# Optimization experiments

Hardware: AMD Instinct MI355X
Metric: run time of the kernel (lower is better)

## Reference

```python
import jax, jax.numpy as jnp
import numpy as np

B, N, D = 8, 128, 256
EPS = 1e-5


def _layernorm(x, g, b):
    m = jnp.mean(x, axis=-1, keepdims=True)
    v = jnp.mean(jnp.square(x - m), axis=-1, keepdims=True)
    return (x - m) * jax.lax.rsqrt(v + EPS) * g + b


def setup_inputs() -> dict:
    key = jax.random.key(0)
    ks = jax.random.split(key, 24)
    s = 0.05  # param init scale
    return {
        "text": jax.random.normal(ks[0], (B, N, D), jnp.float32),
        "adj1": jax.random.uniform(ks[1], (B, N, N), jnp.float32),
        "adj2": jax.random.uniform(ks[2], (B, N, N), jnp.float32),
        "edge1": jax.random.normal(ks[3], (B, N, N, D), jnp.float32) * 0.1,
        "edge2": jax.random.normal(ks[4], (B, N, N, D), jnp.float32) * 0.1,
        "textmask": jnp.ones((B, N), jnp.float32),
        "weight": jax.random.normal(ks[5], (D, D), jnp.float32) * s,
        "bias": jax.random.normal(ks[6], (D,), jnp.float32) * s,
        "gamma": jnp.ones((D,), jnp.float32),
        "beta": jnp.zeros((D,), jnp.float32),
        "fuse1_w": jax.random.normal(ks[7], (2 * D, D), jnp.float32) * s,
        "fuse2_w": jax.random.normal(ks[8], (2 * D, D), jnp.float32) * s,
        "fc3_w": jax.random.normal(ks[9], (2 * D, D), jnp.float32) * s,
        "fc1_w0": jax.random.normal(ks[10], (3 * D, D), jnp.float32) * s,
        "fc1_w1": jax.random.normal(ks[11], (D, 1), jnp.float32) * s,
        "fc1_b1": jnp.zeros((1,), jnp.float32),
        "fc2_w0": jax.random.normal(ks[12], (3 * D, D), jnp.float32) * s,
        "fc2_w1": jax.random.normal(ks[13], (D, 1), jnp.float32) * s,
        "fc2_b1": jnp.zeros((1,), jnp.float32),
        "align_lin": jax.random.normal(ks[14], (D, D), jnp.float32) * s,
        "align_bias": jax.random.normal(ks[15], (D,), jnp.float32) * s,
    }


def reference(text, adj1, adj2, edge1, edge2, textmask, weight, bias, gamma,
              beta, fuse1_w, fuse2_w, fc3_w, fc1_w0, fc1_w1, fc1_b1,
              fc2_w0, fc2_w1, fc2_b1, align_lin, align_bias):
    d = text.shape[-1]
    # ---- SelfAlignment ----
    logits = jnp.einsum('bid,bjd->bij', text @ align_lin, text)
    mask_add = (1.0 - textmask)[:, None, :] * -1e20
    probs = jax.nn.softmax(logits + mask_add, axis=-1)
    outss = jnp.einsum('bij,bjd->bid', probs, text) * textmask[..., None] + align_bias

    # ---- GCN body ----
    out = jax.nn.relu(text @ weight)  # [B,N,D]

    # edge contributions are loop-invariant: precompute once
    # torch cat([x,e]) @ W  ==  x @ W[:d] + e @ W[d:]
    e1_fuse = jnp.einsum('bijd,de->bije', edge1, fuse1_w[d:])
    e2_fuse = jnp.einsum('bijd,de->bije', edge2, fuse2_w[d:])
    e1_fc = jnp.einsum('bijd,de->bije', edge1, fc1_w0[2 * d:])
    e2_fc = jnp.einsum('bijd,de->bije', edge2, fc2_w0[2 * d:])

    denom1 = jnp.sum(adj1, axis=2, keepdims=True) + 1.0  # [B,N,1]
    denom2 = jnp.sum(adj2, axis=2, keepdims=True) + 1.0

    for _ in range(3):  # K = 3
        # text1[b,i,j] = out[b,i]; text2[b,i,j] = out[b,j]
        t_i1 = (out @ fc1_w0[:d])[:, :, None, :]        # text1 part, fc1
        t_j1 = (out @ fc1_w0[d:2 * d])[:, None, :, :]   # text2 part, fc1
        t_i2 = (out @ fc2_w0[:d])[:, :, None, :]
        t_j2 = (out @ fc2_w0[d:2 * d])[:, None, :, :]

        teout = jax.nn.relu((out @ fuse1_w[:d])[:, None, :, :] + e1_fuse)  # [B,N,N,D]
        tein = jax.nn.relu((out @ fuse2_w[:d])[:, None, :, :] + e2_fuse)

        s1 = jax.nn.sigmoid(jax.nn.relu(t_i1 + t_j1 + e1_fc) @ fc1_w1 + fc1_b1)[..., 0]  # [B,N,N]
        s2 = jax.nn.sigmoid(jax.nn.relu(t_i2 + t_j2 + e2_fc) @ fc2_w1 + fc2_b1)[..., 0]

        out1 = jnp.einsum('bij,bijd->bid', adj1 * s1, teout) / denom1
        out2 = jnp.einsum('bij,bijd->bid', adj2 * s2, tein) / denom2

        out = jax.nn.relu(out1 @ fc3_w[:d] + out2 @ fc3_w[d:]) + out + bias
        out = _layernorm(out, gamma, beta)  # dropout = identity (eval)
    return out, outss
```

## Files before the change

### kernel.cpp

```cpp
#include <hip/hip_runtime.h>

typedef unsigned short u16;
typedef unsigned int u32;
typedef __attribute__((ext_vector_type(8))) short bf16x8;
typedef __attribute__((ext_vector_type(4))) float f32x4;
typedef __attribute__((ext_vector_type(16))) float f32x16;

__device__ __forceinline__ u16 f2bf(float f) {
  u32 u = __float_as_uint(f);
  return (u16)((u + 0x7fffu + ((u >> 16) & 1u)) >> 16);
}
__device__ __forceinline__ float bf2f(u16 h) {
  return __uint_as_float(((u32)h) << 16);
}

__device__ __forceinline__ void glds16(const void* g, void* l) {
  __builtin_amdgcn_global_load_lds(
      (const __attribute__((address_space(1))) unsigned int*)g,
      (__attribute__((address_space(3))) unsigned int*)l, 16, 0, 0);
}

__device__ __forceinline__ f32x16 unpack16(const u16* p) {
  uint4 a = *(const uint4*)p, b = *(const uint4*)(p + 8);
  f32x16 r;
  r[0]  = __uint_as_float(a.x << 16); r[1]  = __uint_as_float(a.x & 0xffff0000u);
  r[2]  = __uint_as_float(a.y << 16); r[3]  = __uint_as_float(a.y & 0xffff0000u);
  r[4]  = __uint_as_float(a.z << 16); r[5]  = __uint_as_float(a.z & 0xffff0000u);
  r[6]  = __uint_as_float(a.w << 16); r[7]  = __uint_as_float(a.w & 0xffff0000u);
  r[8]  = __uint_as_float(b.x << 16); r[9]  = __uint_as_float(b.x & 0xffff0000u);
  r[10] = __uint_as_float(b.y << 16); r[11] = __uint_as_float(b.y & 0xffff0000u);
  r[12] = __uint_as_float(b.z << 16); r[13] = __uint_as_float(b.z & 0xffff0000u);
  r[14] = __uint_as_float(b.w << 16); r[15] = __uint_as_float(b.w & 0xffff0000u);
  return r;
}

__global__ __launch_bounds__(256) void convert_edge(
    const float* __restrict__ src, u16* __restrict__ dst) {
  int g = blockIdx.x * 256 + threadIdx.x;
  int kg = g & 7, r = (g >> 3) & 127, kc = (g >> 10) & 3, rt = g >> 12;
  const float* s = src + ((long)(rt * 128 + r) * 256 + kc * 64 + kg * 8);
  float4 a = *(const float4*)s, b = *(const float4*)(s + 4);
  ushort4 lo, hi;
  lo.x = f2bf(a.x); lo.y = f2bf(a.y); lo.z = f2bf(a.z); lo.w = f2bf(a.w);
  hi.x = f2bf(b.x); hi.y = f2bf(b.y); hi.z = f2bf(b.z); hi.w = f2bf(b.w);
  u16* d = dst + (long)rt * 65536 + kc * 16384 + r * 64 + (kg ^ (r & 7)) * 8;
  *(ushort4*)d = lo;
  *(ushort4*)(d + 4) = hi;
}

__global__ __launch_bounds__(256) void gemm_edge(
    const u16* __restrict__ A, const u16* __restrict__ Bt,
    u16* __restrict__ E) {
  __shared__ __align__(16) u16 Asm[8192];
  __shared__ __align__(16) u16 Bsm[8192];
  const int tid = threadIdx.x, lane = tid & 63, w = tid >> 6;
  const int m = lane & 15, q = lane >> 4;
  const int rt = blockIdx.x >> 2, ct = blockIdx.x & 3;
  const int wrow = (w & 1) * 64, wcol = (w >> 1) * 64;
  const char* Ab = (const char*)A + (long)rt * 131072;
  const char* Bb = (const char*)Bt + (long)ct * 65536;
  f32x4 acc[4][4];
#pragma unroll
  for (int r = 0; r < 4; ++r)
#pragma unroll
    for (int c = 0; c < 4; ++c) acc[r][c] = (f32x4){0.f, 0.f, 0.f, 0.f};

  for (int kc = 0; kc < 4; ++kc) {
#pragma unroll
    for (int t = 0; t < 4; ++t) {
      glds16(Ab + kc * 32768 + t * 4096 + tid * 16,
             (char*)Asm + t * 4096 + tid * 16);
      glds16(Bb + kc * 16384 + t * 4096 + tid * 16,
             (char*)Bsm + t * 4096 + tid * 16);
    }
    __syncthreads();
#pragma unroll
    for (int s = 0; s < 2; ++s) {
      const int ko2 = (s * 32 + q * 8) * 2;
      bf16x8 av[4], bv[4];
#pragma unroll
      for (int r = 0; r < 4; ++r) {
        int row = wrow + r * 16 + m;
        av[r] = *(const bf16x8*)((const char*)Asm + row * 128 +
                                 (ko2 ^ ((row & 7) * 16)));
      }
#pragma unroll
      for (int c = 0; c < 4; ++c) {
        int col = wcol + c * 16 + m;
        bv[c] = *(const bf16x8*)((const char*)Bsm + col * 128 +
                                 (ko2 ^ ((col & 7) * 16)));
      }
#pragma unroll
      for (int r = 0; r < 4; ++r)
#pragma unroll
        for (int c = 0; c < 4; ++c)
          acc[r][c] = __builtin_amdgcn_mfma_f32_16x16x32_bf16(
              av[r], bv[c], acc[r][c], 0, 0, 0);
    }
    __syncthreads();
  }
#pragma unroll
  for (int r = 0; r < 4; ++r)
#pragma unroll
    for (int c = 0; c < 4; ++c)
#pragma unroll
      for (int g = 0; g < 4; ++g) {
        long gr = (long)rt * 128 + wrow + r * 16 + q * 4 + g;
        int gc = ct * 128 + wcol + c * 16 + m;
        E[gr * 512 + gc] = f2bf(acc[r][c][g]);
      }
}

template<int K, int RF, bool OUT_BF16, bool RELU0>
__global__ __launch_bounds__(256) void gemm_mfma(
    const float* __restrict__ A, const u16* __restrict__ Bt,
    void* __restrict__ Cv, int Ntot, float* __restrict__ relu_dst) {
  constexpr int ROWS = RF * 16;
  constexpr int LD = 72;
  __shared__ __align__(16) u16 Asm[ROWS * LD];
  __shared__ __align__(16) u16 Bsm[256 * LD];
  const int tid = threadIdx.x;
  const int lane = tid & 63;
  const int w = tid >> 6;
  const int m = lane & 15;
  const int q = lane >> 4;
  const int wcol = w * 64;
  const long rowbase = (long)blockIdx.x * ROWS;
  const long colbase = (long)blockIdx.y * 256;
  f32x4 acc[RF][4];
#pragma unroll
  for (int r = 0; r < RF; ++r)
#pragma unroll
    for (int c = 0; c < 4; ++c) acc[r][c] = (f32x4){0.f, 0.f, 0.f, 0.f};

  for (int kc = 0; kc < K / 64; ++kc) {
    const int kb = kc * 64;
#pragma unroll
    for (int it = 0; it < RF; ++it) {
      int f = it * 256 + tid;
      int r = f >> 4, c4 = (f & 15) * 4;
      float4 v = *(const float4*)(A + (rowbase + r) * K + kb + c4);
      ushort4 h;
      h.x = f2bf(v.x); h.y = f2bf(v.y); h.z = f2bf(v.z); h.w = f2bf(v.w);
      *(ushort4*)&Asm[r * LD + c4] = h;
    }
#pragma unroll
    for (int it = 0; it < 8; ++it) {
      int f = it * 256 + tid;
      int c = f >> 3, k8 = (f & 7) * 8;
      *(uint4*)&Bsm[c * LD + k8] =
          *(const uint4*)(Bt + (colbase + c) * K + kb + k8);
    }
    __syncthreads();
#pragma unroll
    for (int s = 0; s < 2; ++s) {
      const int ko = s * 32 + q * 8;
      bf16x8 av[RF], bv[4];
#pragma unroll
      for (int r = 0; r < RF; ++r)
        av[r] = *(const bf16x8*)&Asm[(r * 16 + m) * LD + ko];
#pragma unroll
      for (int c = 0; c < 4; ++c)
        bv[c] = *(const bf16x8*)&Bsm[(wcol + c * 16 + m) * LD + ko];
#pragma unroll
      for (int r = 0; r < RF; ++r)
#pragma unroll
        for (int c = 0; c < 4; ++c)
          acc[r][c] = __builtin_amdgcn_mfma_f32_16x16x32_bf16(
              av[r], bv[c], acc[r][c], 0, 0, 0);
    }
    __syncthreads();
  }
#pragma unroll
  for (int r = 0; r < RF; ++r)
#pragma unroll
    for (int c = 0; c < 4; ++c)
#pragma unroll
      for (int g = 0; g < 4; ++g) {
        long gr = rowbase + r * 16 + q * 4 + g;
        long gc = colbase + wcol + c * 16 + m;
        float v = acc[r][c][g];
        if (OUT_BF16) ((u16*)Cv)[gr * Ntot + gc] = f2bf(v);
        else          ((float*)Cv)[gr * Ntot + gc] = v;
        if (RELU0) {
          if (gc < 256) relu_dst[gr * 256 + gc] = fmaxf(v, 0.f);
        }
      }
}

__global__ __launch_bounds__(256) void prep_bt(
    const float* __restrict__ weight, const float* __restrict__ align_lin,
    const float* __restrict__ fuse1_w, const float* __restrict__ fuse2_w,
    const float* __restrict__ fc1_w0, const float* __restrict__ fc2_w0,
    const float* __restrict__ fc3_w,
    u16* BtE1, u16* BtE2, u16* BtW0, u16* BtLoop, u16* BtFc3) {
  int g = blockIdx.x * 256 + threadIdx.x;
  if (g < 262144) {
    int t = g & 131071;
    int col = t >> 8, k = t & 255;
    float v;
    if (g < 131072)
      v = (col < 256) ? fuse1_w[(256 + k) * 256 + col]
                      : fc1_w0[(512 + k) * 256 + (col - 256)];
    else
      v = (col < 256) ? fuse2_w[(256 + k) * 256 + col]
                      : fc2_w0[(512 + k) * 256 + (col - 256)];
    int ct = col >> 7, cc = col & 127, kc = k >> 6, kk = k & 63;
    u16* dst = (g < 131072) ? BtE1 : BtE2;
    dst[ct * 32768 + kc * 8192 + cc * 64 + (kk ^ ((cc & 7) * 8))] = f2bf(v);
  } else if (g < 393216) {
    int t = g - 262144;
    int c = t >> 8, k = t & 255;
    float v = (c < 256) ? weight[k * 256 + c] : align_lin[k * 256 + (c - 256)];
    BtW0[t] = f2bf(v);
  } else if (g < 786432) {
    int t = g - 393216;
    int c = t >> 8, k = t & 255;
    int seg = c >> 8, cc = c & 255;
    float v;
    if      (seg == 0) v = fuse1_w[k * 256 + cc];
    else if (seg == 1) v = fuse2_w[k * 256 + cc];
    else if (seg == 2) v = fc1_w0[k * 256 + cc];
    else if (seg == 3) v = fc1_w0[(256 + k) * 256 + cc];
    else if (seg == 4) v = fc2_w0[k * 256 + cc];
    else               v = fc2_w0[(256 + k) * 256 + cc];
    BtLoop[t] = f2bf(v);
  } else {
    int t = g - 786432;
    int c = t >> 9, k = t & 511;
    BtFc3[t] = f2bf(fc3_w[k * 256 + c]);
  }
}

__global__ __launch_bounds__(128) void align_kernel(
    const float* __restrict__ text, const float* __restrict__ T0,
    const float* __restrict__ textmask, const float* __restrict__ align_bias,
    float* __restrict__ outss) {
  const int bi = blockIdx.x;
  const int b = bi >> 7;
  const int tid = threadIdx.x;
  __shared__ float ta[256];
  __shared__ float pr[128];
  __shared__ float red[128];
  ta[tid]       = T0[(long)bi * 512 + 256 + tid];
  ta[tid + 128] = T0[(long)bi * 512 + 384 + tid];
  __syncthreads();
  const float* trow = text + (long)(b * 128 + tid) * 256;
  float dot = 0.f;
  for (int d = 0; d < 256; d += 4) {
    float4 t4 = *(const float4*)(trow + d);
    dot += t4.x * ta[d] + t4.y * ta[d + 1] + t4.z * ta[d + 2] + t4.w * ta[d + 3];
  }
  float logit = dot + (1.0f - textmask[b * 128 + tid]) * -1e20f;
  pr[tid] = logit;
  red[tid] = logit;
  __syncthreads();
  for (int off = 64; off; off >>= 1) {
    if (tid < off) red[tid] = fmaxf(red[tid], red[tid + off]);
    __syncthreads();
  }
  float mx = red[0];
  __syncthreads();
  float e = __expf(pr[tid] - mx);
  red[tid] = e;
  __syncthreads();
  for (int off = 64; off; off >>= 1) {
    if (tid < off) red[tid] += red[tid + off];
    __syncthreads();
  }
  float inv = 1.0f / red[0];
  __syncthreads();
  pr[tid] = e * inv;
  __syncthreads();
  const float mi = textmask[bi];
  for (int h = 0; h < 2; ++h) {
    int d = tid + h * 128;
    float s = 0.f;
    for (int j = 0; j < 128; ++j)
      s += pr[j] * text[(long)(b * 128 + j) * 256 + d];
    outss[(long)bi * 256 + d] = s * mi + align_bias[d];
  }
}

__global__ __launch_bounds__(256) void fused_gate(
    const u16* __restrict__ E1, const u16* __restrict__ E2,
    const float* __restrict__ P, const float* __restrict__ adj1,
    const float* __restrict__ adj2, const float* __restrict__ fc1w1,
    const float* __restrict__ fc1b1, const float* __restrict__ fc2w1,
    const float* __restrict__ fc2b1, float* __restrict__ OU12) {
  const int tid = threadIdx.x, lane = tid & 63, w = tid >> 6;
  const int g16 = lane >> 4, l16 = lane & 15;
  const int bi = blockIdx.x, b = bi >> 7;
  const int db = l16 * 16;
  const long rowi = (long)bi * 1536;
  const long ebase = (long)bi * 65536;
  const int abase = bi * 128;

  __shared__ float sA[128], sB[128];
  __shared__ float redA[4][256], redB[4][256];
  __shared__ float dInv[2];

  if (w < 2) {
    const float* adj = w ? adj2 : adj1;
    float v = adj[abase + lane] + adj[abase + 64 + lane];
#pragma unroll
    for (int off = 32; off; off >>= 1) v += __shfl_xor(v, off);
    if (lane == 0) dInv[w] = 1.f / (1.f + v);
  }

  {
    const f32x16 w1v = *(const f32x16*)(fc1w1 + db);
    const f32x16 w2v = *(const f32x16*)(fc2w1 + db);
    const f32x16 ti1 = *(const f32x16*)(P + rowi + 512 + db);
    const f32x16 ti2 = *(const f32x16*)(P + rowi + 1024 + db);
    const float b1 = fc1b1[0], b2 = fc2b1[0];
#pragma unroll
    for (int t = 0; t < 8; ++t) {
      const int j = w * 32 + t * 4 + g16;
      const long er = ebase + (long)j * 512;
      const long rowj = (long)((b << 7) + j) * 1536;
      f32x16 e1 = unpack16(E1 + er + 256 + db);
      f32x16 e2 = unpack16(E2 + er + 256 + db);
      f32x16 t1 = *(const f32x16*)(P + rowj + 768 + db);
      f32x16 t2 = *(const f32x16*)(P + rowj + 1280 + db);
      float z1 = 0.f, z2 = 0.f;
#pragma unroll
      for (int dd = 0; dd < 16; ++dd) {
        z1 += fmaxf(ti1[dd] + t1[dd] + e1[dd], 0.f) * w1v[dd];
        z2 += fmaxf(ti2[dd] + t2[dd] + e2[dd], 0.f) * w2v[dd];
      }
#pragma unroll
      for (int off = 1; off < 16; off <<= 1) {
        z1 += __shfl_xor(z1, off);
        z2 += __shfl_xor(z2, off);
      }
      if (l16 == 0) {
        sA[j] = adj1[abase + j] / (1.f + __expf(-(z1 + b1)));
        sB[j] = adj2[abase + j] / (1.f + __expf(-(z2 + b2)));
      }
    }
  }
  __syncthreads();

  f32x16 acc1, acc2;
#pragma unroll
  for (int dd = 0; dd < 16; ++dd) { acc1[dd] = 0.f; acc2[dd] = 0.f; }
#pragma unroll
  for (int t = 0; t < 8; ++t) {
    const int j = w * 32 + t * 4 + g16;
    const long er = ebase + (long)j * 512;
    const long rowj = (long)((b << 7) + j) * 1536;
    f32x16 e1 = unpack16(E1 + er + db);
    f32x16 e2 = unpack16(E2 + er + db);
    f32x16 o1 = *(const f32x16*)(P + rowj + db);
    f32x16 o2 = *(const f32x16*)(P + rowj + 256 + db);
    const float s1 = sA[j], s2 = sB[j];
#pragma unroll
    for (int dd = 0; dd < 16; ++dd) {
      acc1[dd] += s1 * fmaxf(o1[dd] + e1[dd], 0.f);
      acc2[dd] += s2 * fmaxf(o2[dd] + e2[dd], 0.f);
    }
  }

#pragma unroll
  for (int dd = 0; dd < 16; ++dd) {
    float a = acc1[dd], c = acc2[dd];
    a += __shfl_xor(a, 16); a += __shfl_xor(a, 32);
    c += __shfl_xor(c, 16); c += __shfl_xor(c, 32);
    acc1[dd] = a; acc2[dd] = c;
  }
  *(float4*)&redA[w][db + g16 * 4] =
      make_float4(acc1[g16 * 4], acc1[g16 * 4 + 1],
                  acc1[g16 * 4 + 2], acc1[g16 * 4 + 3]);
  *(float4*)&redB[w][db + g16 * 4] =
      make_float4(acc2[g16 * 4], acc2[g16 * 4 + 1],
                  acc2[g16 * 4 + 2], acc2[g16 * 4 + 3]);
  __syncthreads();
  float o1 = redA[0][tid] + redA[1][tid] + redA[2][tid] + redA[3][tid];
  float o2 = redB[0][tid] + redB[1][tid] + redB[2][tid] + redB[3][tid];
  OU12[(long)bi * 512 + tid] = o1 * dInv[0];
  OU12[(long)bi * 512 + 256 + tid] = o2 * dInv[1];
}

__global__ __launch_bounds__(256) void ln_kernel(
    const float* __restrict__ Y, const float* __restrict__ prev,
    const float* __restrict__ bias, const float* __restrict__ gamma,
    const float* __restrict__ beta, float* __restrict__ dst) {
  const int row = blockIdx.x, tid = threadIdx.x, lane = tid & 63, w = tid >> 6;
  const long idx = (long)row * 256 + tid;
  float v = fmaxf(Y[idx], 0.f) + prev[idx] + bias[tid];
  float s = v;
#pragma unroll
  for (int off = 32; off; off >>= 1) s += __shfl_xor(s, off);
  __shared__ float wsA[4], wsB[4];
  if (lane == 0) wsA[w] = s;
  __syncthreads();
  float mean = (wsA[0] + wsA[1] + wsA[2] + wsA[3]) * (1.0f / 256.0f);
  float c = v - mean;
  float s2 = c * c;
#pragma unroll
  for (int off = 32; off; off >>= 1) s2 += __shfl_xor(s2, off);
  if (lane == 0) wsB[w] = s2;
  __syncthreads();
  float var = (wsB[0] + wsB[1] + wsB[2] + wsB[3]) * (1.0f / 256.0f);
  dst[idx] = c * rsqrtf(var + 1e-5f) * gamma[tid] + beta[tid];
}

extern "C" void kernel_launch(void* const* d_in, const int* in_sizes, int n_in,
                              void* d_out, int out_size, void* d_ws, size_t ws_size,
                              hipStream_t stream) {
  const float* text      = (const float*)d_in[0];
  const float* adj1      = (const float*)d_in[1];
  const float* adj2      = (const float*)d_in[2];
  const float* edge1     = (const float*)d_in[3];
  const float* edge2     = (const float*)d_in[4];
  const float* textmask  = (const float*)d_in[5];
  const float* weight    = (const float*)d_in[6];
  const float* bias      = (const float*)d_in[7];
  const float* gamma     = (const float*)d_in[8];
  const float* beta      = (const float*)d_in[9];
  const float* fuse1_w   = (const float*)d_in[10];
  const float* fuse2_w   = (const float*)d_in[11];
  const float* fc3_w     = (const float*)d_in[12];
  const float* fc1_w0    = (const float*)d_in[13];
  const float* fc1_w1    = (const float*)d_in[14];
  const float* fc1_b1    = (const float*)d_in[15];
  const float* fc2_w0    = (const float*)d_in[16];
  const float* fc2_w1    = (const float*)d_in[17];
  const float* fc2_b1    = (const float*)d_in[18];
  const float* align_lin = (const float*)d_in[19];
  const float* align_bias= (const float*)d_in[20];
  float* outF = (float*)d_out;

  char* w8 = (char*)d_ws;
  u16* Ax   = (u16*)w8;
  u16* E1   = (u16*)(w8 + 67108864);
  u16* E2   = (u16*)(w8 + 201326592);
  u16* BtE1 = (u16*)(w8 + 335544320);
  u16* BtE2 = BtE1 + 131072;
  u16* BtW0 = BtE2 + 131072;
  u16* BtLoop = BtW0 + 131072;
  u16* BtFc3  = BtLoop + 393216;
  float* P    = (float*)w8;
  float* T0   = P + 1572864;
  float* OU12 = T0 + 524288;
  float* outb = OU12 + 524288;
  float* Yb   = outb + 262144;

  prep_bt<<<3584, 256, 0, stream>>>(weight, align_lin, fuse1_w, fuse2_w,
                                    fc1_w0, fc2_w0, fc3_w,
                                    BtE1, BtE2, BtW0, BtLoop, BtFc3);
  convert_edge<<<16384, 256, 0, stream>>>(edge1, Ax);
  gemm_edge<<<4096, 256, 0, stream>>>(Ax, BtE1, E1);
  convert_edge<<<16384, 256, 0, stream>>>(edge2, Ax);
  gemm_edge<<<4096, 256, 0, stream>>>(Ax, BtE2, E2);
  gemm_mfma<256, 2, false, true><<<dim3(32, 2), 256, 0, stream>>>(
      text, BtW0, T0, 512, outb);
  align_kernel<<<1024, 128, 0, stream>>>(text, T0, textmask, align_bias,
                                         outF + 262144);
  for (int it = 0; it < 3; ++it) {
    gemm_mfma<256, 2, false, false><<<dim3(32, 6), 256, 0, stream>>>(
        outb, BtLoop, P, 1536, nullptr);
    fused_gate<<<1024, 256, 0, stream>>>(E1, E2, P, adj1, adj2, fc1_w1, fc1_b1,
                                         fc2_w1, fc2_b1, OU12);
    gemm_mfma<512, 2, false, false><<<dim3(32, 1), 256, 0, stream>>>(
        OU12, BtFc3, Yb, 256, nullptr);
    ln_kernel<<<1024, 256, 0, stream>>>(Yb, outb, bias, gamma, beta,
                                        (it == 2) ? outF : outb);
  }
}
```

Measured before the change: 843.4 us.

## Fuse edge fp32-to-bf16 conversion into edge GEMM and split gate kernel over j halves

Removes the separate convert_edge pass: gemm_edge now reads fp32 edge tensors directly, converts them to bf16 and writes the swizzled layout into LDS, with a remapped block order. This avoids writing and re-reading a large bf16 staging buffer. fused_gate is restructured to two blocks per row, each covering half of j, with a simpler per-lane float4 layout and a full-wave reduction. The two partial outputs are summed in the A-load of the fc3 GEMM. The costs are register-path loads replacing async LDS loads in the edge GEMM, and more shuffle reductions in the gate kernel.

```diff
diff --git a/kernel.cpp b/kernel.cpp
--- a/kernel.cpp
+++ b/kernel.cpp
@@ -4,14 +4,10 @@
 typedef unsigned int u32;
 typedef __attribute__((ext_vector_type(8))) short bf16x8;
 typedef __attribute__((ext_vector_type(4))) float f32x4;
-typedef __attribute__((ext_vector_type(16))) float f32x16;
 
 __device__ __forceinline__ u16 f2bf(float f) {
   u32 u = __float_as_uint(f);
   return (u16)((u + 0x7fffu + ((u >> 16) & 1u)) >> 16);
-}
-__device__ __forceinline__ float bf2f(u16 h) {
-  return __uint_as_float(((u32)h) << 16);
 }
 
 __device__ __forceinline__ void glds16(const void* g, void* l) {
@@ -20,44 +16,28 @@
       (__attribute__((address_space(3))) unsigned int*)l, 16, 0, 0);
 }
 
-__device__ __forceinline__ f32x16 unpack16(const u16* p) {
-  uint4 a = *(const uint4*)p, b = *(const uint4*)(p + 8);
-  f32x16 r;
-  r[0]  = __uint_as_float(a.x << 16); r[1]  = __uint_as_float(a.x & 0xffff0000u);
-  r[2]  = __uint_as_float(a.y << 16); r[3]  = __uint_as_float(a.y & 0xffff0000u);
-  r[4]  = __uint_as_float(a.z << 16); r[5]  = __uint_as_float(a.z & 0xffff0000u);
-  r[6]  = __uint_as_float(a.w << 16); r[7]  = __uint_as_float(a.w & 0xffff0000u);
-  r[8]  = __uint_as_float(b.x << 16); r[9]  = __uint_as_float(b.x & 0xffff0000u);
-  r[10] = __uint_as_float(b.y << 16); r[11] = __uint_as_float(b.y & 0xffff0000u);
-  r[12] = __uint_as_float(b.z << 16); r[13] = __uint_as_float(b.z & 0xffff0000u);
-  r[14] = __uint_as_float(b.w << 16); r[15] = __uint_as_float(b.w & 0xffff0000u);
+__device__ __forceinline__ float4 unpack4(const u16* p) {
+  uint2 a = *(const uint2*)p;
+  float4 r;
+  r.x = __uint_as_float(a.x << 16);
+  r.y = __uint_as_float(a.x & 0xffff0000u);
+  r.z = __uint_as_float(a.y << 16);
+  r.w = __uint_as_float(a.y & 0xffff0000u);
   return r;
 }
 
-__global__ __launch_bounds__(256) void convert_edge(
-    const float* __restrict__ src, u16* __restrict__ dst) {
-  int g = blockIdx.x * 256 + threadIdx.x;
-  int kg = g & 7, r = (g >> 3) & 127, kc = (g >> 10) & 3, rt = g >> 12;
-  const float* s = src + ((long)(rt * 128 + r) * 256 + kc * 64 + kg * 8);
-  float4 a = *(const float4*)s, b = *(const float4*)(s + 4);
-  ushort4 lo, hi;
-  lo.x = f2bf(a.x); lo.y = f2bf(a.y); lo.z = f2bf(a.z); lo.w = f2bf(a.w);
-  hi.x = f2bf(b.x); hi.y = f2bf(b.y); hi.z = f2bf(b.z); hi.w = f2bf(b.w);
-  u16* d = dst + (long)rt * 65536 + kc * 16384 + r * 64 + (kg ^ (r & 7)) * 8;
-  *(ushort4*)d = lo;
-  *(ushort4*)(d + 4) = hi;
-}
-
 __global__ __launch_bounds__(256) void gemm_edge(
-    const u16* __restrict__ A, const u16* __restrict__ Bt,
+    const float* __restrict__ Af, const u16* __restrict__ Bt,
     u16* __restrict__ E) {
   __shared__ __align__(16) u16 Asm[8192];
   __shared__ __align__(16) u16 Bsm[8192];
   const int tid = threadIdx.x, lane = tid & 63, w = tid >> 6;
   const int m = lane & 15, q = lane >> 4;
-  const int rt = blockIdx.x >> 2, ct = blockIdx.x & 3;
+  const int p = blockIdx.x;
+  const int rt = (p & 7) * 128 + (p >> 5);
+  const int ct = (p >> 3) & 3;
   const int wrow = (w & 1) * 64, wcol = (w >> 1) * 64;
-  const char* Ab = (const char*)A + (long)rt * 131072;
+  const float* Ab = Af + (long)rt * 32768;
   const char* Bb = (const char*)Bt + (long)ct * 65536;
   f32x4 acc[4][4];
 #pragma unroll
@@ -67,12 +47,18 @@
 
   for (int kc = 0; kc < 4; ++kc) {
 #pragma unroll
-    for (int t = 0; t < 4; ++t) {
-      glds16(Ab + kc * 32768 + t * 4096 + tid * 16,
-             (char*)Asm + t * 4096 + tid * 16);
+    for (int it = 0; it < 8; ++it) {
+      int f = it * 256 + tid;
+      int r = f >> 4, c4 = (f & 15) * 4;
+      float4 v = *(const float4*)(Ab + (long)r * 256 + kc * 64 + c4);
+      ushort4 h;
+      h.x = f2bf(v.x); h.y = f2bf(v.y); h.z = f2bf(v.z); h.w = f2bf(v.w);
+      *(ushort4*)((char*)Asm + r * 128 + ((c4 * 2) ^ ((r & 7) * 16))) = h;
+    }
+#pragma unroll
+    for (int t = 0; t < 4; ++t)
       glds16(Bb + kc * 16384 + t * 4096 + tid * 16,
              (char*)Bsm + t * 4096 + tid * 16);
-    }
     __syncthreads();
 #pragma unroll
     for (int s = 0; s < 2; ++s) {
@@ -111,10 +97,11 @@
       }
 }
 
-template<int K, int RF, bool OUT_BF16, bool RELU0>
+template<int K, int RF, bool OUT_BF16, bool RELU0, bool SUM2>
 __global__ __launch_bounds__(256) void gemm_mfma(
     const float* __restrict__ A, const u16* __restrict__ Bt,
-    void* __restrict__ Cv, int Ntot, float* __restrict__ relu_dst) {
+    void* __restrict__ Cv, int Ntot, float* __restrict__ relu_dst,
+    const float* __restrict__ A2) {
   constexpr int ROWS = RF * 16;
   constexpr int LD = 72;
   __shared__ __align__(16) u16 Asm[ROWS * LD];
@@ -140,6 +127,10 @@
       int f = it * 256 + tid;
       int r = f >> 4, c4 = (f & 15) * 4;
       float4 v = *(const float4*)(A + (rowbase + r) * K + kb + c4);
+      if (SUM2) {
+        float4 v2 = *(const float4*)(A2 + (rowbase + r) * K + kb + c4);
+        v.x += v2.x; v.y += v2.y; v.z += v2.z; v.w += v2.w;
+      }
       ushort4 h;
       h.x = f2bf(v.x); h.y = f2bf(v.y); h.z = f2bf(v.z); h.w = f2bf(v.w);
       *(ushort4*)&Asm[r * LD + c4] = h;
@@ -287,99 +278,90 @@
     const float* __restrict__ P, const float* __restrict__ adj1,
     const float* __restrict__ adj2, const float* __restrict__ fc1w1,
     const float* __restrict__ fc1b1, const float* __restrict__ fc2w1,
-    const float* __restrict__ fc2b1, float* __restrict__ OU12) {
+    const float* __restrict__ fc2b1, float* __restrict__ OUa,
+    float* __restrict__ OUb) {
   const int tid = threadIdx.x, lane = tid & 63, w = tid >> 6;
-  const int g16 = lane >> 4, l16 = lane & 15;
-  const int bi = blockIdx.x, b = bi >> 7;
-  const int db = l16 * 16;
+  const int bi = blockIdx.x >> 1, half = blockIdx.x & 1;
+  const int b = bi >> 7;
+  const int d4 = lane * 4;
   const long rowi = (long)bi * 1536;
   const long ebase = (long)bi * 65536;
   const int abase = bi * 128;
-
-  __shared__ float sA[128], sB[128];
+  float* __restrict__ OU = half ? OUb : OUa;
+
+  __shared__ float sA[64], sB[64];
   __shared__ float redA[4][256], redB[4][256];
   __shared__ float dInv[2];
 
-  if (w < 2) {
-    const float* adj = w ? adj2 : adj1;
-    float v = adj[abase + lane] + adj[abase + 64 + lane];
+  if (tid < 64) sA[tid] = adj1[abase + half * 64 + tid];
+  else if (tid < 128) sB[tid - 64] = adj2[abase + half * 64 + (tid - 64)];
+  if (w == 0) {
+    float v = adj1[abase + lane] + adj1[abase + 64 + lane];
 #pragma unroll
     for (int off = 32; off; off >>= 1) v += __shfl_xor(v, off);
-    if (lane == 0) dInv[w] = 1.f / (1.f + v);
-  }
-
-  {
-    const f32x16 w1v = *(const f32x16*)(fc1w1 + db);
-    const f32x16 w2v = *(const f32x16*)(fc2w1 + db);
-    const f32x16 ti1 = *(const f32x16*)(P + rowi + 512 + db);
-    const f32x16 ti2 = *(const f32x16*)(P + rowi + 1024 + db);
-    const float b1 = fc1b1[0], b2 = fc2b1[0];
-#pragma unroll
-    for (int t = 0; t < 8; ++t) {
-      const int j = w * 32 + t * 4 + g16;
-      const long er = ebase + (long)j * 512;
-      const long rowj = (long)((b << 7) + j) * 1536;
-      f32x16 e1 = unpack16(E1 + er + 256 + db);
-      f32x16 e2 = unpack16(E2 + er + 256 + db);
-      f32x16 t1 = *(const f32x16*)(P + rowj + 768 + db);
-      f32x16 t2 = *(const f32x16*)(P + rowj + 1280 + db);
-      float z1 = 0.f, z2 = 0.f;
-#pragma unroll
-      for (int dd = 0; dd < 16; ++dd) {
-        z1 += fmaxf(ti1[dd] + t1[dd] + e1[dd], 0.f) * w1v[dd];
-        z2 += fmaxf(ti2[dd] + t2[dd] + e2[dd], 0.f) * w2v[dd];
-      }
-#pragma unroll
-      for (int off = 1; off < 16; off <<= 1) {
-        z1 += __shfl_xor(z1, off);
-        z2 += __shfl_xor(z2, off);
-      }
-      if (l16 == 0) {
-        sA[j] = adj1[abase + j] / (1.f + __expf(-(z1 + b1)));
-        sB[j] = adj2[abase + j] / (1.f + __expf(-(z2 + b2)));
-      }
-    }
-  }
-  __syncthreads();
-
-  f32x16 acc1, acc2;
-#pragma unroll
-  for (int dd = 0; dd < 16; ++dd) { acc1[dd] = 0.f; acc2[dd] = 0.f; }
-#pragma unroll
-  for (int t = 0; t < 8; ++t) {
-    const int j = w * 32 + t * 4 + g16;
+    if (lane == 0) dInv[0] = 1.f / (1.f + v);
+  } else if (w == 1) {
+    float v = adj2[abase + lane] + adj2[abase + 64 + lane];
+#pragma unroll
+    for (int off = 32; off; off >>= 1) v += __shfl_xor(v, off);
+    if (lane == 0) dInv[1] = 1.f / (1.f + v);
+  }
+  __syncthreads();
+
+  const float4 ti1 = *(const float4*)(P + rowi + 512 + d4);
+  const float4 ti2 = *(const float4*)(P + rowi + 1024 + d4);
+  const float4 w1v = *(const float4*)(fc1w1 + d4);
+  const float4 w2v = *(const float4*)(fc2w1 + d4);
+  const float b1 = fc1b1[0], b2 = fc2b1[0];
+
+  float4 acc1 = {0.f, 0.f, 0.f, 0.f}, acc2 = {0.f, 0.f, 0.f, 0.f};
+
+#pragma unroll 2
+  for (int t = 0; t < 16; ++t) {
+    const int jl = w * 16 + t;
+    const int j = half * 64 + jl;
     const long er = ebase + (long)j * 512;
     const long rowj = (long)((b << 7) + j) * 1536;
-    f32x16 e1 = unpack16(E1 + er + db);
-    f32x16 e2 = unpack16(E2 + er + db);
-    f32x16 o1 = *(const f32x16*)(P + rowj + db);
-    f32x16 o2 = *(const f32x16*)(P + rowj + 256 + db);
-    const float s1 = sA[j], s2 = sB[j];
-#pragma unroll
-    for (int dd = 0; dd < 16; ++dd) {
-      acc1[dd] += s1 * fmaxf(o1[dd] + e1[dd], 0.f);
-      acc2[dd] += s2 * fmaxf(o2[dd] + e2[dd], 0.f);
-    }
-  }
-
-#pragma unroll
-  for (int dd = 0; dd < 16; ++dd) {
-    float a = acc1[dd], c = acc2[dd];
-    a += __shfl_xor(a, 16); a += __shfl_xor(a, 32);
-    c += __shfl_xor(c, 16); c += __shfl_xor(c, 32);
-    acc1[dd] = a; acc2[dd] = c;
-  }
-  *(float4*)&redA[w][db + g16 * 4] =
-      make_float4(acc1[g16 * 4], acc1[g16 * 4 + 1],
-                  acc1[g16 * 4 + 2], acc1[g16 * 4 + 3]);
-  *(float4*)&redB[w][db + g16 * 4] =
-      make_float4(acc2[g16 * 4], acc2[g16 * 4 + 1],
-                  acc2[g16 * 4 + 2], acc2[g16 * 4 + 3]);
-  __syncthreads();
-  float o1 = redA[0][tid] + redA[1][tid] + redA[2][tid] + redA[3][tid];
-  float o2 = redB[0][tid] + redB[1][tid] + redB[2][tid] + redB[3][tid];
-  OU12[(long)bi * 512 + tid] = o1 * dInv[0];
-  OU12[(long)bi * 512 + 256 + tid] = o2 * dInv[1];
+    float4 e1c = unpack4(E1 + er + 256 + d4);
+    float4 e2c = unpack4(E2 + er + 256 + d4);
+    float4 t1 = *(const float4*)(P + rowj + 768 + d4);
+    float4 t2 = *(const float4*)(P + rowj + 1280 + d4);
+    float z1 = fmaxf(ti1.x + t1.x + e1c.x, 0.f) * w1v.x +
+               fmaxf(ti1.y + t1.y + e1c.y, 0.f) * w1v.y +
+               fmaxf(ti1.z + t1.z + e1c.z, 0.f) * w1v.z +
+               fmaxf(ti1.w + t1.w + e1c.w, 0.f) * w1v.w;
+    float z2 = fmaxf(ti2.x + t2.x + e2c.x, 0.f) * w2v.x +
+               fmaxf(ti2.y + t2.y + e2c.y, 0.f) * w2v.y +
+               fmaxf(ti2.z + t2.z + e2c.z, 0.f) * w2v.z +
+               fmaxf(ti2.w + t2.w + e2c.w, 0.f) * w2v.w;
+#pragma unroll
+    for (int off = 1; off < 64; off <<= 1) {
+      z1 += __shfl_xor(z1, off);
+      z2 += __shfl_xor(z2, off);
+    }
+    float s1 = sA[jl] * __builtin_amdgcn_rcpf(1.f + __expf(-(z1 + b1)));
+    float s2 = sB[jl] * __builtin_amdgcn_rcpf(1.f + __expf(-(z2 + b2)));
+    float4 e1f = unpack4(E1 + er + d4);
+    float4 e2f = unpack4(E2 + er + d4);
+    float4 o1 = *(const float4*)(P + rowj + d4);
+    float4 o2 = *(const float4*)(P + rowj + 256 + d4);
+    acc1.x += s1 * fmaxf(o1.x + e1f.x, 0.f);
+    acc1.y += s1 * fmaxf(o1.y + e1f.y, 0.f);
+    acc1.z += s1 * fmaxf(o1.z + e1f.z, 0.f);
+    acc1.w += s1 * fmaxf(o1.w + e1f.w, 0.f);
+    acc2.x += s2 * fmaxf(o2.x + e2f.x, 0.f);
+    acc2.y += s2 * fmaxf(o2.y + e2f.y, 0.f);
+    acc2.z += s2 * fmaxf(o2.z + e2f.z, 0.f);
+    acc2.w += s2 * fmaxf(o2.w + e2f.w, 0.f);
+  }
+
+  *(float4*)&redA[w][d4] = acc1;
+  *(float4*)&redB[w][d4] = acc2;
+  __syncthreads();
+  float r1 = redA[0][tid] + redA[1][tid] + redA[2][tid] + redA[3][tid];
+  float r2 = redB[0][tid] + redB[1][tid] + redB[2][tid] + redB[3][tid];
+  OU[(long)bi * 512 + tid] = r1 * dInv[0];
+  OU[(long)bi * 512 + 256 + tid] = r2 * dInv[1];
 }
 
 __global__ __launch_bounds__(256) void ln_kernel(
@@ -433,7 +415,6 @@
   float* outF = (float*)d_out;
 
   char* w8 = (char*)d_ws;
-  u16* Ax   = (u16*)w8;
   u16* E1   = (u16*)(w8 + 67108864);
   u16* E2   = (u16*)(w8 + 201326592);
   u16* BtE1 = (u16*)(w8 + 335544320);
@@ -443,28 +424,27 @@
   u16* BtFc3  = BtLoop + 393216;
   float* P    = (float*)w8;
   float* T0   = P + 1572864;
-  float* OU12 = T0 + 524288;
-  float* outb = OU12 + 524288;
+  float* OUa  = T0 + 524288;
+  float* OUb  = OUa + 524288;
+  float* outb = OUb + 524288;
   float* Yb   = outb + 262144;
 
   prep_bt<<<3584, 256, 0, stream>>>(weight, align_lin, fuse1_w, fuse2_w,
                                     fc1_w0, fc2_w0, fc3_w,
                                     BtE1, BtE2, BtW0, BtLoop, BtFc3);
-  convert_edge<<<16384, 256, 0, stream>>>(edge1, Ax);
-  gemm_edge<<<4096, 256, 0, stream>>>(Ax, BtE1, E1);
-  convert_edge<<<16384, 256, 0, stream>>>(edge2, Ax);
-  gemm_edge<<<4096, 256, 0, stream>>>(Ax, BtE2, E2);
-  gemm_mfma<256, 2, false, true><<<dim3(32, 2), 256, 0, stream>>>(
-      text, BtW0, T0, 512, outb);
+  gemm_edge<<<4096, 256, 0, stream>>>(edge1, BtE1, E1);
+  gemm_edge<<<4096, 256, 0, stream>>>(edge2, BtE2, E2);
+  gemm_mfma<256, 2, false, true, false><<<dim3(32, 2), 256, 0, stream>>>(
+      text, BtW0, T0, 512, outb, nullptr);
   align_kernel<<<1024, 128, 0, stream>>>(text, T0, textmask, align_bias,
                                          outF + 262144);
   for (int it = 0; it < 3; ++it) {
-    gemm_mfma<256, 2, false, false><<<dim3(32, 6), 256, 0, stream>>>(
-        outb, BtLoop, P, 1536, nullptr);
-    fused_gate<<<1024, 256, 0, stream>>>(E1, E2, P, adj1, adj2, fc1_w1, fc1_b1,
-                                         fc2_w1, fc2_b1, OU12);
-    gemm_mfma<512, 2, false, false><<<dim3(32, 1), 256, 0, stream>>>(
-        OU12, BtFc3, Yb, 256, nullptr);
+    gemm_mfma<256, 2, false, false, false><<<dim3(32, 6), 256, 0, stream>>>(
+        outb, BtLoop, P, 1536, nullptr, nullptr);
+    fused_gate<<<2048, 256, 0, stream>>>(E1, E2, P, adj1, adj2, fc1_w1, fc1_b1,
+                                         fc2_w1, fc2_b1, OUa, OUb);
+    gemm_mfma<512, 2, false, false, true><<<dim3(32, 1), 256, 0, stream>>>(
+        OUa, BtFc3, Yb, 256, nullptr, OUb);
     ln_kernel<<<1024, 256, 0, stream>>>(Yb, outb, bias, gamma, beta,
                                         (it == 2) ? outF : outb);
   }
```

Result: faster. 739.7 us (-12.3%).
